# Kernel tuning notes

Hardware: AMD Instinct MI355X
Metric: run time of the kernel (lower is better)

The kernel has to match this reference:

```python
import jax, jax.numpy as jnp
import numpy as np

B, T, IN, H, Z, DH, K = 512, 256, 5, 256, 128, 512, 20
OUT = 6 * K + 3


def setup_inputs() -> dict:
    key = jax.random.key(0)
    ks = jax.random.split(key, 24)
    p = lambda k, shp: jax.random.normal(k, shp, dtype=jnp.float32) * 0.05
    return {
        "s": jax.random.normal(ks[0], (B, T, IN), dtype=jnp.float32),
        "epsilon": jax.random.normal(ks[1], (Z,), dtype=jnp.float32),
        "Wih_f": p(ks[2], (4 * H, IN)), "Whh_f": p(ks[3], (4 * H, H)),
        "bih_f": p(ks[4], (4 * H,)), "bhh_f": p(ks[5], (4 * H,)),
        "Wih_b": p(ks[6], (4 * H, IN)), "Whh_b": p(ks[7], (4 * H, H)),
        "bih_b": p(ks[8], (4 * H,)), "bhh_b": p(ks[9], (4 * H,)),
        "W_sigma": p(ks[10], (Z, 2 * H)), "b_sigma": p(ks[11], (Z,)),
        "W_mu": p(ks[12], (Z, 2 * H)), "b_mu": p(ks[13], (Z,)),
        "W_h0": p(ks[14], (DH, Z)), "b_h0": p(ks[15], (DH,)),
        "Wih_d": p(ks[16], (4 * DH, IN + Z)), "Whh_d": p(ks[17], (4 * DH, DH)),
        "bih_d": p(ks[18], (4 * DH,)), "bhh_d": p(ks[19], (4 * DH,)),
        "W_dec": p(ks[20], (OUT, DH)), "b_dec": p(ks[21], (OUT,)),
    }


def _lstm_scan(x, Wih, Whh, b, reverse):
    # x: [T, B, in]; PyTorch gate order i, f, g, o
    Hh = Whh.shape[1]
    h0 = jnp.zeros((x.shape[1], Hh), x.dtype)

    def step(carry, xt):
        h, c = carry
        g = xt @ Wih.T + h @ Whh.T + b
        i, f, gg, o = jnp.split(g, 4, axis=-1)
        c = jax.nn.sigmoid(f) * c + jax.nn.sigmoid(i) * jnp.tanh(gg)
        h = jax.nn.sigmoid(o) * jnp.tanh(c)
        return (h, c), h

    _, hs = jax.lax.scan(step, (h0, h0), x, reverse=reverse)
    return hs  # [T, B, Hh]


def _mdn(y):
    # y: [..., 123] -> per-mixture (pi, mu1, mu2, sx, sy, corr) + 3 pen logits
    mix = y[..., :6 * K].reshape(y.shape[:-1] + (K, 6))
    pi = jax.nn.softmax(mix[..., 0], axis=-1)
    out_mix = jnp.stack(
        [pi, mix[..., 1], mix[..., 2], jnp.exp(mix[..., 3]),
         jnp.exp(mix[..., 4]), jnp.tanh(mix[..., 5])], axis=-1)
    pen = jax.nn.softmax(y[..., 6 * K:], axis=-1)
    return jnp.concatenate([out_mix.reshape(y.shape[:-1] + (6 * K,)), pen], axis=-1)


def reference(s, epsilon, Wih_f, Whh_f, bih_f, bhh_f, Wih_b, Whh_b, bih_b, bhh_b,
              W_sigma, b_sigma, W_mu, b_mu, W_h0, b_h0,
              Wih_d, Whh_d, bih_d, bhh_d, W_dec, b_dec):
    x = jnp.transpose(s, (1, 0, 2))  # [T, B, 5]
    hf = _lstm_scan(x, Wih_f, Whh_f, bih_f + bhh_f, False)
    hb = _lstm_scan(x, Wih_b, Whh_b, bih_b + bhh_b, True)
    h = jnp.concatenate([hf[-1], hb[-1]], axis=-1)  # output at last time step, [B, 512]
    presig = h @ W_sigma.T + b_sigma
    mu = h @ W_mu.T + b_mu
    sigma = jnp.exp(presig / 2)
    z = mu + sigma * epsilon  # [B, Z]
    h0 = jnp.tanh(z @ W_h0.T + b_h0)
    c0 = jnp.zeros((s.shape[0], DH), s.dtype)
    s0 = jnp.tile(jnp.array([0.0, 0.0, 1.0, 0.0, 0.0], s.dtype), (s.shape[0], 1))
    dec_in = jnp.concatenate([s0[None], x[:T - 1]], axis=0)  # [T, B, 5]
    bdec = bih_d + bhh_d

    def step(carry, st):
        hh, cc = carry
        xt = jnp.concatenate([st, z], axis=-1)  # [B, 133]
        g = xt @ Wih_d.T + hh @ Whh_d.T + bdec
        i, f, gg, o = jnp.split(g, 4, axis=-1)
        cc = jax.nn.sigmoid(f) * cc + jax.nn.sigmoid(i) * jnp.tanh(gg)
        hh = jax.nn.sigmoid(o) * jnp.tanh(cc)
        y = hh @ W_dec.T + b_dec
        return (hh, cc), y

    _, ys = jax.lax.scan(step, (h0, c0), dec_in)  # [T, B, 123]
    output = _mdn(jnp.transpose(ys, (1, 0, 2)))   # [B, T, 123]
    return (output, mu, presig)
```

## Files before the change

### kernel.cpp

```cpp
#include <hip/hip_runtime.h>

typedef unsigned short u16;
typedef unsigned long long u64;
typedef __attribute__((ext_vector_type(8))) short bfrag;
typedef __attribute__((ext_vector_type(4))) float f32x4;

#define MFMA __builtin_amdgcn_mfma_f32_16x16x32_bf16

#define OFF_FLAGS 0ull
#define OFF_HENC  4096ull
#define OFF_WENC  528384ull
#define OFF_WDEC  1118208ull
#define OFF_WY    3870720ull
#define OFF_WMS   4001792ull
#define OFF_WH0   4280320ull
#define OFF_HDEC  4444160ull
#define OFF_HLAT  5492736ull
#define OFF_MS    6049792ull
#define OFF_AZ    6574080ull

__device__ __forceinline__ u16 f2bf(float f) {
  union { float f; unsigned int i; } v; v.f = f;
  unsigned int r = v.i + 0x7fffu + ((v.i >> 16) & 1u);
  return (u16)(r >> 16);
}
__device__ __forceinline__ float sigm(float x) { return 1.0f / (1.0f + __expf(-x)); }
__device__ __forceinline__ float tanh_(float x) {
  float a = fabsf(x);
  float e = __expf(-2.0f * a);
  float r = (1.0f - e) / (1.0f + e);
  return x < 0.0f ? -r : r;
}

__device__ __forceinline__ u64 aload(const u64* p) {
  return __hip_atomic_load(p, __ATOMIC_RELAXED, __HIP_MEMORY_SCOPE_AGENT);
}
__device__ __forceinline__ void astore(u64* p, u64 v) {
  __hip_atomic_store(p, v, __ATOMIC_RELAXED, __HIP_MEMORY_SCOPE_AGENT);
}
__device__ __forceinline__ float afload(const float* p) {
  return __hip_atomic_load(p, __ATOMIC_RELAXED, __HIP_MEMORY_SCOPE_AGENT);
}
__device__ __forceinline__ void afstore(float* p, float v) {
  __hip_atomic_store(p, v, __ATOMIC_RELAXED, __HIP_MEMORY_SCOPE_AGENT);
}

__device__ __forceinline__ void gwait(int* flags, int g, int ep, int tid, int* sdead) {
  if (ep > 0) {
    if (tid < 32 && *sdead == 0) {
      int* fp = flags + g * 64 + tid;
      int spin = 0;
      while (__hip_atomic_load(fp, __ATOMIC_RELAXED, __HIP_MEMORY_SCOPE_AGENT) < ep) {
        __builtin_amdgcn_s_sleep(1);
        if (++spin > (1 << 20)) { *sdead = 1; break; }
      }
    }
  }
  __syncthreads();
  asm volatile("" ::: "memory");
}
__device__ __forceinline__ void garrive(int* flags, int g, int m, int ep, int tid) {
  asm volatile("s_waitcnt vmcnt(0)" ::: "memory");
  __syncthreads();
  if (tid == 0)
    __hip_atomic_store(flags + g * 64 + m, ep, __ATOMIC_RELAXED, __HIP_MEMORY_SCOPE_AGENT);
}

__global__ void pack_wenc(const float* __restrict__ Whh, const float* __restrict__ Wih,
                          const float* __restrict__ bi, const float* __restrict__ bh,
                          u16* __restrict__ out) {
  int idx = blockIdx.x * 256 + threadIdx.x;
  if (idx >= 294912) return;
  int m = idx / 9216, within = idx % 9216;
  int kb = within >> 10, rest = within & 1023;
  int ng = rest >> 9, l = (rest >> 3) & 63, j = rest & 7;
  int nl = ng * 16 + (l & 15);
  int u = nl >> 2, g = nl & 3;
  int row = g * 256 + m * 8 + u;
  int k = kb * 32 + (l >> 4) * 8 + j;
  float v = 0.f;
  if (k < 256) v = Whh[row * 256 + k];
  else if (k < 261) v = Wih[row * 5 + (k - 256)];
  else if (k == 261) v = bi[row] + bh[row];
  out[idx] = f2bf(v);
}

__global__ void pack_wdec(const float* __restrict__ Whh, const float* __restrict__ Wih,
                          const float* __restrict__ bi, const float* __restrict__ bh,
                          u16* __restrict__ out) {
  int idx = blockIdx.x * 256 + threadIdx.x;
  if (idx >= 1376256) return;
  int m = idx / 43008, within = idx % 43008;
  int kb = within >> 11, rest = within & 2047;
  int w = rest >> 9, l = (rest >> 3) & 63, j = rest & 7;
  int nl = w * 16 + (l & 15);
  int u = nl >> 2, g = nl & 3;
  int row = g * 512 + m * 16 + u;
  int k = kb * 32 + (l >> 4) * 8 + j;
  float v = 0.f;
  if (k < 512) v = Whh[row * 512 + k];
  else if (k < 640) v = Wih[row * 133 + 5 + (k - 512)];
  else if (k < 645) v = Wih[row * 133 + (k - 640)];
  else if (k == 645) v = bi[row] + bh[row];
  out[idx] = f2bf(v);
}

__global__ void pack_wy(const float* __restrict__ Wd, u16* __restrict__ out) {
  int idx = blockIdx.x * 256 + threadIdx.x;
  if (idx >= 65536) return;
  int m = idx >> 13, within = idx & 8191;
  int kb = within >> 9, rest = within & 511;
  int l = rest >> 3, j = rest & 7;
  int row = m * 16 + (l & 15);
  int k = kb * 32 + (l >> 4) * 8 + j;
  float v = (row < 123 && k < 512) ? Wd[row * 512 + k] : 0.f;
  out[idx] = f2bf(v);
}

__global__ void pack_wms(const float* __restrict__ Wmu, const float* __restrict__ bmu,
                         const float* __restrict__ Wsig, const float* __restrict__ bsig,
                         u16* __restrict__ out) {
  int idx = blockIdx.x * 256 + threadIdx.x;
  if (idx >= 139264) return;
  int r = idx / 544, k = idx % 544;
  float v = 0.f;
  if (r < 128) {
    if (k < 512) v = Wmu[r * 512 + k];
    else if (k == 512) v = bmu[r];
  } else {
    int r2 = r - 128;
    if (k < 512) v = Wsig[r2 * 512 + k];
    else if (k == 512) v = bsig[r2];
  }
  out[idx] = f2bf(v);
}

__global__ void pack_wh0(const float* __restrict__ Wh0, const float* __restrict__ bh0,
                         u16* __restrict__ out) {
  int idx = blockIdx.x * 256 + threadIdx.x;
  if (idx >= 81920) return;
  int r = idx / 160, k = idx % 160;
  float v = 0.f;
  if (k < 128) v = Wh0[r * 128 + k];
  else if (k == 128) v = bh0[r];
  out[idx] = f2bf(v);
}

__global__ __launch_bounds__(256, 1) void rnn_persist(
    int* __restrict__ flags, u16* __restrict__ henc,
    const u16* __restrict__ WENCP, const u16* __restrict__ WDECP,
    const u16* __restrict__ WYP, const u16* __restrict__ WMSP, const u16* __restrict__ WH0P,
    u16* __restrict__ hdec, u16* __restrict__ hlat, float* __restrict__ msbuf,
    u16* __restrict__ Az,
    const float* __restrict__ s, const float* __restrict__ eps,
    const float* __restrict__ Wih_b, const float* __restrict__ bih_b,
    const float* __restrict__ bhh_b,
    const float* __restrict__ b_dec, float* __restrict__ out)
{
  __shared__ __align__(16) u16 sm[72960];
  __shared__ __align__(16) float gbuf[2112];
  __shared__ __align__(16) u16 hst[1024];
  __shared__ int sdead;

  const int tid = threadIdx.x;
  const int blk = blockIdx.x;
  const int g = blk & 7;
  const int m = blk >> 3;
  const int B0 = g * 64;
  const int w = tid >> 6, l = tid & 63;
  const int lr = l & 15, ko = (l >> 4) * 8;

  float* out_mu = out + 16121856;
  float* out_ps = out + 16187392;

  const int gcol = m * 16 + lr;
  float bd = 0.f;
  if (m < 8 && gcol < 123) bd = b_dec[gcol];

  if (tid == 0) sdead = 0;
  {
    bfrag zz = {0, 0, 0, 0, 0, 0, 0, 0};
    #pragma unroll
    for (int i = 0; i < 5; ++i) {
      int c = i * 256 + tid;
      if (c < 1184) *(bfrag*)(sm + c * 8) = zz;
    }
  }
  {
    const u16* src = WENCP + (size_t)m * 9216;
    #pragma unroll
    for (int i = 0; i < 5; ++i) {
      int c = i * 256 + tid;
      if (c < 1152) *(bfrag*)(sm + 21760 + c * 8) = *(const bfrag*)(src + c * 8);
    }
  }
  __syncthreads();
  if (tid < 32) sm[tid * 296 + 261] = 0x3F80;
  __syncthreads();

  float c_enc0 = 0.f, c_enc1 = 0.f;
  #pragma unroll 1
  for (int t = 0; t < 256; ++t) {
    gwait(flags, g, t, tid, &sdead);
    const u64* hs0 = (const u64*)(henc + (size_t)((t + 1) & 1) * 131072 + (size_t)B0 * 256);
    u64 hv0[8], hv1[8];
    #pragma unroll
    for (int i = 0; i < 8; ++i) hv0[i] = aload(hs0 + i * 256 + tid);
    #pragma unroll
    for (int i = 0; i < 8; ++i) hv1[i] = aload(hs0 + 2048 + i * 256 + tid);
    #pragma unroll
    for (int hh = 0; hh < 2; ++hh) {
      #pragma unroll
      for (int i = 0; i < 8; ++i) {
        int idx = i * 256 + tid;
        *(u64*)(sm + (idx >> 6) * 296 + (idx & 63) * 4) = (hh == 0) ? hv0[i] : hv1[i];
      }
      if (tid < 32) {
        const float* xr = s + ((size_t)(B0 + hh * 32 + tid) * 256 + t) * 5;
        #pragma unroll
        for (int j = 0; j < 5; ++j) sm[tid * 296 + 256 + j] = f2bf(xr[j]);
      }
      __syncthreads();
      const int mt = w >> 1, ng = w & 1;
      f32x4 acc = {0.f, 0.f, 0.f, 0.f};
      #pragma unroll
      for (int kb = 0; kb < 9; ++kb) {
        bfrag a = *(const bfrag*)(sm + (mt * 16 + lr) * 296 + kb * 32 + ko);
        bfrag bw = *(const bfrag*)(sm + 21760 + (kb * 2 + ng) * 512 + l * 8);
        acc = MFMA(a, bw, acc, 0, 0, 0);
      }
      #pragma unroll
      for (int j = 0; j < 4; ++j)
        gbuf[(mt * 16 + (l >> 4) * 4 + j) * 33 + ng * 16 + lr] = acc[j];
      __syncthreads();
      {
        int bl = tid >> 3, u = tid & 7;
        float gi = gbuf[bl * 33 + u * 4 + 0], gf = gbuf[bl * 33 + u * 4 + 1];
        float gg = gbuf[bl * 33 + u * 4 + 2], go = gbuf[bl * 33 + u * 4 + 3];
        float cprev = (hh == 0) ? c_enc0 : c_enc1;
        float c = sigm(gf) * cprev + sigm(gi) * tanh_(gg);
        if (hh == 0) c_enc0 = c; else c_enc1 = c;
        hst[bl * 8 + u] = f2bf(sigm(go) * tanh_(c));
      }
      __syncthreads();
      if (tid < 64) {
        int row = tid >> 1, q = tid & 1;
        u64 v = *(const u64*)(hst + row * 8 + q * 4);
        astore((u64*)(henc + (size_t)(t & 1) * 131072 + (size_t)(B0 + hh * 32 + row) * 256 + m * 8) + q, v);
      }
    }
    garrive(flags, g, m, t + 1, tid);
  }

  u16* lat_hf = (u16*)gbuf;
  u16* lat_hb = (u16*)gbuf + 512;
  u16* lat_z  = (u16*)gbuf + 1024;

  gwait(flags, g, 256, tid, &sdead);
  {
    const u16* src = WDECP + (size_t)m * 43008;
    #pragma unroll 1
    for (int i = 0; i < 21; ++i) {
      int c = i * 256 + tid;
      *(bfrag*)(sm + 21760 + c * 8) = *(const bfrag*)(src + c * 8);
    }
  }
  if (m < 8) {
    const u16* src = WYP + (size_t)m * 8192;
    #pragma unroll
    for (int i = 0; i < 4; ++i) {
      int c = i * 256 + tid;
      *(bfrag*)(sm + 64768 + c * 8) = *(const bfrag*)(src + c * 8);
    }
  }
  #pragma unroll
  for (int r = 0; r < 2; ++r) {
    int b = B0 + m * 2 + r;
    if (tid < 64) {
      u64 v = aload((const u64*)(henc + 131072 + (size_t)b * 256) + tid);
      *(u64*)(lat_hf + r * 256 + tid * 4) = v;
    }
    {
      const float* xr = s + ((size_t)b * 256 + 255) * 5;
      float x0 = xr[0], x1 = xr[1], x2 = xr[2], x3 = xr[3], x4 = xr[4];
      int n = tid;
      float gv[4];
      #pragma unroll
      for (int gg = 0; gg < 4; ++gg) {
        int row = gg * 256 + n;
        gv[gg] = bih_b[row] + bhh_b[row] + x0 * Wih_b[row * 5] + x1 * Wih_b[row * 5 + 1] +
                 x2 * Wih_b[row * 5 + 2] + x3 * Wih_b[row * 5 + 3] + x4 * Wih_b[row * 5 + 4];
      }
      float c = sigm(gv[0]) * tanh_(gv[2]);
      lat_hb[r * 256 + n] = f2bf(sigm(gv[3]) * tanh_(c));
    }
  }
  __syncthreads();
  #pragma unroll
  for (int it = 0; it < 2; ++it) {
    int idx = it * 256 + tid;
    if (idx < 272) {
      int rr = idx / 136, u = idx % 136;
      u64 pv = 0;
      #pragma unroll
      for (int q = 0; q < 4; ++q) {
        int c = u * 4 + q;
        u16 x;
        if (c < 256) x = lat_hf[rr * 256 + c];
        else if (c < 512) x = lat_hb[rr * 256 + c - 256];
        else if (c == 512) x = 0x3F80;
        else x = 0;
        pv |= ((u64)x) << (q * 16);
      }
      astore((u64*)(hlat + (size_t)(B0 + m * 2 + rr) * 544) + u, pv);
    }
  }
  garrive(flags, g, m, 257, tid);

  gwait(flags, g, 257, tid, &sdead);
  {
    const int bH = m >> 4, cT = m & 15;
    const u64* src = (const u64*)(hlat + (size_t)(B0 + bH * 32) * 544);
    u64 sv[17];
    #pragma unroll
    for (int i = 0; i < 17; ++i) sv[i] = aload(src + i * 256 + tid);
    #pragma unroll
    for (int i = 0; i < 17; ++i) *(u64*)(sm + (i * 256 + tid) * 4) = sv[i];
    __syncthreads();
    if (w < 2) {
      f32x4 acc = {0.f, 0.f, 0.f, 0.f};
      const u16* bp = WMSP + (size_t)(cT * 16 + lr) * 544 + ko;
      #pragma unroll
      for (int kb = 0; kb < 17; ++kb) {
        bfrag a = *(const bfrag*)(sm + (w * 16 + lr) * 544 + kb * 32 + ko);
        bfrag bb = *(const bfrag*)(bp + kb * 32);
        acc = MFMA(a, bb, acc, 0, 0, 0);
      }
      int nc = cT * 16 + lr;
      #pragma unroll
      for (int j = 0; j < 4; ++j) {
        int b = B0 + bH * 32 + w * 16 + (l >> 4) * 4 + j;
        afstore(msbuf + (size_t)b * 256 + nc, acc[j]);
        if (nc < 128) out_mu[(size_t)b * 128 + nc] = acc[j];
        else out_ps[(size_t)b * 128 + nc - 128] = acc[j];
      }
    }
  }
  garrive(flags, g, m, 258, tid);

  gwait(flags, g, 258, tid, &sdead);
  {
    int r = tid >> 7, zj = tid & 127;
    int b = B0 + m * 2 + r;
    float mu = afload(msbuf + (size_t)b * 256 + zj);
    float ps = afload(msbuf + (size_t)b * 256 + 128 + zj);
    float z = mu + __expf(0.5f * ps) * eps[zj];
    lat_z[r * 128 + zj] = f2bf(z);
  }
  __syncthreads();
  if (tid < 80) {
    int r = tid / 40, u = tid % 40;
    u64 pv = 0;
    #pragma unroll
    for (int q = 0; q < 4; ++q) {
      int c = u * 4 + q;
      u16 x;
      if (c < 128) x = lat_z[r * 128 + c];
      else if (c == 128) x = 0x3F80;
      else x = 0;
      pv |= ((u64)x) << (q * 16);
    }
    astore((u64*)(Az + (size_t)(B0 + m * 2 + r) * 160) + u, pv);
  }
  garrive(flags, g, m, 259, tid);

  gwait(flags, g, 259, tid, &sdead);
  u64 zreg0[4], zreg1[4];
  {
    int r = tid >> 3;
    #pragma unroll
    for (int i = 0; i < 4; ++i) {
      int uu = (tid & 7) * 4 + i;
      zreg0[i] = aload((const u64*)(Az + (size_t)(B0 + r) * 160) + uu);
      zreg1[i] = aload((const u64*)(Az + (size_t)(B0 + 32 + r) * 160) + uu);
    }
  }
  {
    const u64* src = (const u64*)(Az + (size_t)B0 * 160);
    u64 sv[10];
    #pragma unroll
    for (int i = 0; i < 10; ++i) sv[i] = aload(src + i * 256 + tid);
    #pragma unroll
    for (int i = 0; i < 10; ++i) *(u64*)(sm + (i * 256 + tid) * 4) = sv[i];
    __syncthreads();
    f32x4 acc = {0.f, 0.f, 0.f, 0.f};
    const u16* bp = WH0P + (size_t)(m * 16 + lr) * 160 + ko;
    #pragma unroll
    for (int kb = 0; kb < 5; ++kb) {
      bfrag a = *(const bfrag*)(sm + (w * 16 + lr) * 160 + kb * 32 + ko);
      bfrag bb = *(const bfrag*)(bp + kb * 32);
      acc = MFMA(a, bb, acc, 0, 0, 0);
    }
    #pragma unroll
    for (int j = 0; j < 4; ++j)
      hst[(w * 16 + (l >> 4) * 4 + j) * 16 + lr] = f2bf(tanh_(acc[j]));
  }
  __syncthreads();
  #pragma unroll
  for (int i = 0; i < 5; ++i) {
    int idx = i * 256 + tid;
    if (idx < 1120) {
      int row = idx / 35, c = idx % 35;
      sm[row * 680 + 645 + c] = (c == 0) ? 0x3F80 : 0;
    }
  }
  {
    int row = tid >> 2, q = tid & 3;
    u64 v = *(const u64*)(hst + row * 16 + q * 4);
    astore((u64*)(hdec + 262144 + (size_t)(B0 + row) * 512 + m * 16) + q, v);
  }
  garrive(flags, g, m, 260, tid);

  float c_dec00 = 0.f, c_dec01 = 0.f, c_dec10 = 0.f, c_dec11 = 0.f;
  #pragma unroll 1
  for (int t = 0; t < 256; ++t) {
    gwait(flags, g, 260 + t, tid, &sdead);
    const u64* hs0 = (const u64*)(hdec + (size_t)((t + 1) & 1) * 262144 + (size_t)B0 * 512);
    u64 hv0[16], hv1[16];
    #pragma unroll
    for (int i = 0; i < 16; ++i) hv0[i] = aload(hs0 + i * 256 + tid);
    #pragma unroll
    for (int i = 0; i < 16; ++i) hv1[i] = aload(hs0 + 4096 + i * 256 + tid);
    #pragma unroll
    for (int hh = 0; hh < 2; ++hh) {
      #pragma unroll
      for (int i = 0; i < 16; ++i) {
        int idx = i * 256 + tid;
        *(u64*)(sm + (idx >> 7) * 680 + (idx & 127) * 4) = (hh == 0) ? hv0[i] : hv1[i];
      }
      {
        int r = tid >> 3;
        #pragma unroll
        for (int i = 0; i < 4; ++i) {
          int uu = (tid & 7) * 4 + i;
          *(u64*)(sm + r * 680 + 512 + uu * 4) = (hh == 0) ? zreg0[i] : zreg1[i];
        }
      }
      if (tid < 32) {
        if (t == 0) {
          sm[tid * 680 + 640] = 0; sm[tid * 680 + 641] = 0; sm[tid * 680 + 642] = 0x3F80;
          sm[tid * 680 + 643] = 0; sm[tid * 680 + 644] = 0;
        } else {
          const float* xr = s + ((size_t)(B0 + hh * 32 + tid) * 256 + (t - 1)) * 5;
          #pragma unroll
          for (int j = 0; j < 5; ++j) sm[tid * 680 + 640 + j] = f2bf(xr[j]);
        }
      }
      __syncthreads();
      const int mtd = w & 1, nb = (w >> 1) * 2;
      const bool doy = (m < 8) && (w < 2) && (t > 0);
      f32x4 acc0 = {0.f, 0.f, 0.f, 0.f}, acc1 = {0.f, 0.f, 0.f, 0.f}, accy = {0.f, 0.f, 0.f, 0.f};
      #pragma unroll
      for (int kb = 0; kb < 21; ++kb) {
        bfrag a  = *(const bfrag*)(sm + (mtd * 16 + lr) * 680 + kb * 32 + ko);
        bfrag b0 = *(const bfrag*)(sm + 21760 + kb * 2048 + nb * 512 + l * 8);
        bfrag b1 = *(const bfrag*)(sm + 21760 + kb * 2048 + (nb + 1) * 512 + l * 8);
        acc0 = MFMA(a, b0, acc0, 0, 0, 0);
        acc1 = MFMA(a, b1, acc1, 0, 0, 0);
        if (kb < 16 && doy) {
          bfrag by = *(const bfrag*)(sm + 64768 + kb * 512 + l * 8);
          accy = MFMA(a, by, accy, 0, 0, 0);
        }
      }
      if (doy && gcol < 123) {
        int brow = B0 + hh * 32 + w * 16 + (l >> 4) * 4;
        #pragma unroll
        for (int j = 0; j < 4; ++j)
          out[((size_t)(brow + j) * 256 + (t - 1)) * 123 + gcol] = accy[j] + bd;
      }
      #pragma unroll
      for (int j = 0; j < 4; ++j) {
        int grow = mtd * 16 + (l >> 4) * 4 + j;
        gbuf[grow * 66 + nb * 16 + lr] = acc0[j];
        gbuf[grow * 66 + (nb + 1) * 16 + lr] = acc1[j];
      }
      __syncthreads();
      #pragma unroll
      for (int p = 0; p < 2; ++p) {
        int idx = p * 256 + tid;
        int bl = idx >> 4, u = idx & 15;
        float gi = gbuf[bl * 66 + u * 4 + 0], gf = gbuf[bl * 66 + u * 4 + 1];
        float gg = gbuf[bl * 66 + u * 4 + 2], go = gbuf[bl * 66 + u * 4 + 3];
        float cprev = (hh == 0) ? (p == 0 ? c_dec00 : c_dec01) : (p == 0 ? c_dec10 : c_dec11);
        float c = sigm(gf) * cprev + sigm(gi) * tanh_(gg);
        if (hh == 0) { if (p == 0) c_dec00 = c; else c_dec01 = c; }
        else         { if (p == 0) c_dec10 = c; else c_dec11 = c; }
        hst[bl * 16 + u] = f2bf(sigm(go) * tanh_(c));
      }
      __syncthreads();
      if (tid < 128) {
        int row = tid >> 2, q = tid & 3;
        u64 v = *(const u64*)(hst + row * 16 + q * 4);
        astore((u64*)(hdec + (size_t)(t & 1) * 262144 + (size_t)(B0 + hh * 32 + row) * 512 + m * 16) + q, v);
      }
    }
    garrive(flags, g, m, 261 + t, tid);
  }

  gwait(flags, g, 516, tid, &sdead);
  #pragma unroll
  for (int hh = 0; hh < 2; ++hh) {
    const u64* hsrc = (const u64*)(hdec + 262144 + (size_t)(B0 + hh * 32) * 512);
    u64 hv[16];
    #pragma unroll
    for (int i = 0; i < 16; ++i) hv[i] = aload(hsrc + i * 256 + tid);
    #pragma unroll
    for (int i = 0; i < 16; ++i) {
      int idx = i * 256 + tid;
      *(u64*)(sm + (idx >> 7) * 680 + (idx & 127) * 4) = hv[i];
    }
    __syncthreads();
    if (m < 8 && w < 2) {
      f32x4 accy = {0.f, 0.f, 0.f, 0.f};
      #pragma unroll
      for (int kb = 0; kb < 16; ++kb) {
        bfrag a = *(const bfrag*)(sm + (w * 16 + lr) * 680 + kb * 32 + ko);
        bfrag by = *(const bfrag*)(sm + 64768 + kb * 512 + l * 8);
        accy = MFMA(a, by, accy, 0, 0, 0);
      }
      if (gcol < 123) {
        int brow = B0 + hh * 32 + w * 16 + (l >> 4) * 4;
        #pragma unroll
        for (int j = 0; j < 4; ++j)
          out[((size_t)(brow + j) * 256 + 255) * 123 + gcol] = accy[j] + bd;
      }
    }
    __syncthreads();
  }
}

__global__ __launch_bounds__(64) void mdn_final(float* __restrict__ out) {
  __shared__ float rows[64 * 123];
  const int tid = threadIdx.x;
  float4* g4 = (float4*)(out + (size_t)blockIdx.x * 64 * 123);
  #pragma unroll
  for (int i = 0; i < 31; ++i) {
    int c = i * 64 + tid;
    if (c < 1968) ((float4*)rows)[c] = g4[c];
  }
  __syncthreads();
  {
    float* r = rows + tid * 123;
    float m1 = -1e30f;
    #pragma unroll
    for (int k = 0; k < 20; ++k) m1 = fmaxf(m1, r[6 * k]);
    float s1 = 0.f;
    #pragma unroll
    for (int k = 0; k < 20; ++k) s1 += __expf(r[6 * k] - m1);
    float i1 = 1.f / s1;
    #pragma unroll
    for (int k = 0; k < 20; ++k) {
      r[6 * k] = __expf(r[6 * k] - m1) * i1;
      r[6 * k + 3] = __expf(r[6 * k + 3]);
      r[6 * k + 4] = __expf(r[6 * k + 4]);
      r[6 * k + 5] = tanh_(r[6 * k + 5]);
    }
    float p0 = r[120], p1 = r[121], p2 = r[122];
    float mp = fmaxf(p0, fmaxf(p1, p2));
    float e0 = __expf(p0 - mp), e1 = __expf(p1 - mp), e2 = __expf(p2 - mp);
    float ip = 1.f / (e0 + e1 + e2);
    r[120] = e0 * ip; r[121] = e1 * ip; r[122] = e2 * ip;
  }
  __syncthreads();
  #pragma unroll
  for (int i = 0; i < 31; ++i) {
    int c = i * 64 + tid;
    if (c < 1968) g4[c] = ((float4*)rows)[c];
  }
}

extern "C" void kernel_launch(void* const* d_in, const int* in_sizes, int n_in,
                              void* d_out, int out_size, void* d_ws, size_t ws_size,
                              hipStream_t stream) {
  const float* s       = (const float*)d_in[0];
  const float* eps     = (const float*)d_in[1];
  const float* Wih_f   = (const float*)d_in[2];
  const float* Whh_f   = (const float*)d_in[3];
  const float* bih_f   = (const float*)d_in[4];
  const float* bhh_f   = (const float*)d_in[5];
  const float* Wih_b   = (const float*)d_in[6];
  const float* bih_b   = (const float*)d_in[8];
  const float* bhh_b   = (const float*)d_in[9];
  const float* W_sigma = (const float*)d_in[10];
  const float* b_sigma = (const float*)d_in[11];
  const float* W_mu    = (const float*)d_in[12];
  const float* b_mu    = (const float*)d_in[13];
  const float* W_h0    = (const float*)d_in[14];
  const float* b_h0    = (const float*)d_in[15];
  const float* Wih_d   = (const float*)d_in[16];
  const float* Whh_d   = (const float*)d_in[17];
  const float* bih_d   = (const float*)d_in[18];
  const float* bhh_d   = (const float*)d_in[19];
  const float* W_dec   = (const float*)d_in[20];
  const float* b_dec   = (const float*)d_in[21];

  char* ws = (char*)d_ws;
  int* FLAGS  = (int*)(ws + OFF_FLAGS);
  u16* HENC   = (u16*)(ws + OFF_HENC);
  u16* WENCP  = (u16*)(ws + OFF_WENC);
  u16* WDECP  = (u16*)(ws + OFF_WDEC);
  u16* WYP    = (u16*)(ws + OFF_WY);
  u16* WMSP   = (u16*)(ws + OFF_WMS);
  u16* WH0P   = (u16*)(ws + OFF_WH0);
  u16* HDEC   = (u16*)(ws + OFF_HDEC);
  u16* HLAT   = (u16*)(ws + OFF_HLAT);
  float* MS   = (float*)(ws + OFF_MS);
  u16* AZ     = (u16*)(ws + OFF_AZ);
  float* out  = (float*)d_out;

  hipMemsetAsync(ws, 0, 4096 + 524288, stream);

  pack_wenc<<<1152, 256, 0, stream>>>(Whh_f, Wih_f, bih_f, bhh_f, WENCP);
  pack_wdec<<<5376, 256, 0, stream>>>(Whh_d, Wih_d, bih_d, bhh_d, WDECP);
  pack_wy<<<256, 256, 0, stream>>>(W_dec, WYP);
  pack_wms<<<544, 256, 0, stream>>>(W_mu, b_mu, W_sigma, b_sigma, WMSP);
  pack_wh0<<<320, 256, 0, stream>>>(W_h0, b_h0, WH0P);

  rnn_persist<<<256, 256, 0, stream>>>(FLAGS, HENC, WENCP, WDECP, WYP, WMSP, WH0P,
                                       HDEC, HLAT, MS, AZ, s, eps,
                                       Wih_b, bih_b, bhh_b, b_dec, out);

  mdn_final<<<2048, 64, 0, stream>>>(out);

  (void)in_sizes; (void)n_in; (void)out_size; (void)ws_size;
}
```

Measured before the change: 2.984 ms.

## Split per-group barrier into two half-batch flags and prepack bf16 inputs

The cross-block barrier for each batch group is split into two independent flag sets, one per 32-row half. Each half can wait, compute and arrive on its own, so one half's sync latency can overlap the other half's compute in both the encoder and decoder recurrences. A new pre-kernel packs the input sequence into bf16 rows of 8 with a bias-one column, replacing per-step scalar fp32 loads and conversions with single 64-bit loads. The mu/sigma scratch buffer is dropped in favour of reading the output arrays directly, and the spin timeout is shortened, which adds flag-ordering complexity and some risk of deadlock-detection misfires.

```diff
diff --git a/kernel.cpp b/kernel.cpp
--- a/kernel.cpp
+++ b/kernel.cpp
@@ -16,8 +16,8 @@
 #define OFF_WH0   4280320ull
 #define OFF_HDEC  4444160ull
 #define OFF_HLAT  5492736ull
-#define OFF_MS    6049792ull
-#define OFF_AZ    6574080ull
+#define OFF_AZ    6049792ull
+#define OFF_SX    6213632ull
 
 __device__ __forceinline__ u16 f2bf(float f) {
   union { float f; unsigned int i; } v; v.f = f;
@@ -45,25 +45,25 @@
   __hip_atomic_store(p, v, __ATOMIC_RELAXED, __HIP_MEMORY_SCOPE_AGENT);
 }
 
-__device__ __forceinline__ void gwait(int* flags, int g, int ep, int tid, int* sdead) {
+__device__ __forceinline__ void gwait(int* base, int ep, int tid, int* sdead) {
   if (ep > 0) {
     if (tid < 32 && *sdead == 0) {
-      int* fp = flags + g * 64 + tid;
+      int* fp = base + tid;
       int spin = 0;
       while (__hip_atomic_load(fp, __ATOMIC_RELAXED, __HIP_MEMORY_SCOPE_AGENT) < ep) {
         __builtin_amdgcn_s_sleep(1);
-        if (++spin > (1 << 20)) { *sdead = 1; break; }
+        if (++spin > (1 << 18)) { *sdead = 1; break; }
       }
     }
   }
   __syncthreads();
   asm volatile("" ::: "memory");
 }
-__device__ __forceinline__ void garrive(int* flags, int g, int m, int ep, int tid) {
+__device__ __forceinline__ void garrive(int* base, int m, int ep, int tid) {
   asm volatile("s_waitcnt vmcnt(0)" ::: "memory");
   __syncthreads();
   if (tid == 0)
-    __hip_atomic_store(flags + g * 64 + m, ep, __ATOMIC_RELAXED, __HIP_MEMORY_SCOPE_AGENT);
+    __hip_atomic_store(base + m, ep, __ATOMIC_RELAXED, __HIP_MEMORY_SCOPE_AGENT);
 }
 
 __global__ void pack_wenc(const float* __restrict__ Whh, const float* __restrict__ Wih,
@@ -146,12 +146,22 @@
   out[idx] = f2bf(v);
 }
 
+__global__ void pack_sx(const float* __restrict__ s, u16* __restrict__ out) {
+  int idx = blockIdx.x * 256 + threadIdx.x;
+  if (idx >= 1048576) return;
+  int j = idx & 7, b = (idx >> 3) & 511, t = idx >> 12;
+  u16 v;
+  if (j < 5) v = f2bf(s[((size_t)b * 256 + t) * 5 + j]);
+  else v = (j == 5) ? (u16)0x3F80 : (u16)0;
+  out[idx] = v;
+}
+
 __global__ __launch_bounds__(256, 1) void rnn_persist(
     int* __restrict__ flags, u16* __restrict__ henc,
     const u16* __restrict__ WENCP, const u16* __restrict__ WDECP,
     const u16* __restrict__ WYP, const u16* __restrict__ WMSP, const u16* __restrict__ WH0P,
-    u16* __restrict__ hdec, u16* __restrict__ hlat, float* __restrict__ msbuf,
-    u16* __restrict__ Az,
+    u16* __restrict__ hdec, u16* __restrict__ hlat, u16* __restrict__ Az,
+    const u16* __restrict__ SXD,
     const float* __restrict__ s, const float* __restrict__ eps,
     const float* __restrict__ Wih_b, const float* __restrict__ bih_b,
     const float* __restrict__ bhh_b,
@@ -169,6 +179,8 @@
   const int B0 = g * 64;
   const int w = tid >> 6, l = tid & 63;
   const int lr = l & 15, ko = (l >> 4) * 8;
+  int* FA = flags + g * 128;
+  int* FB = FA + 64;
 
   float* out_mu = out + 16121856;
   float* out_ps = out + 16187392;
@@ -195,30 +207,28 @@
     }
   }
   __syncthreads();
-  if (tid < 32) sm[tid * 296 + 261] = 0x3F80;
-  __syncthreads();
 
   float c_enc0 = 0.f, c_enc1 = 0.f;
   #pragma unroll 1
   for (int t = 0; t < 256; ++t) {
-    gwait(flags, g, t, tid, &sdead);
-    const u64* hs0 = (const u64*)(henc + (size_t)((t + 1) & 1) * 131072 + (size_t)B0 * 256);
-    u64 hv0[8], hv1[8];
-    #pragma unroll
-    for (int i = 0; i < 8; ++i) hv0[i] = aload(hs0 + i * 256 + tid);
-    #pragma unroll
-    for (int i = 0; i < 8; ++i) hv1[i] = aload(hs0 + 2048 + i * 256 + tid);
-    #pragma unroll
-    for (int hh = 0; hh < 2; ++hh) {
+    #pragma unroll
+    for (int X = 0; X < 2; ++X) {
+      int* F = X ? FB : FA;
+      gwait(F, t, tid, &sdead);
+      const u64* hs = (const u64*)(henc + (size_t)((t + 1) & 1) * 131072 +
+                                   (size_t)(B0 + X * 32) * 256);
+      u64 hv[8];
+      #pragma unroll
+      for (int i = 0; i < 8; ++i) hv[i] = aload(hs + i * 256 + tid);
       #pragma unroll
       for (int i = 0; i < 8; ++i) {
         int idx = i * 256 + tid;
-        *(u64*)(sm + (idx >> 6) * 296 + (idx & 63) * 4) = (hh == 0) ? hv0[i] : hv1[i];
-      }
-      if (tid < 32) {
-        const float* xr = s + ((size_t)(B0 + hh * 32 + tid) * 256 + t) * 5;
-        #pragma unroll
-        for (int j = 0; j < 5; ++j) sm[tid * 296 + 256 + j] = f2bf(xr[j]);
+        *(u64*)(sm + (idx >> 6) * 296 + (idx & 63) * 4) = hv[i];
+      }
+      if (tid < 64) {
+        int row = tid >> 1, q = tid & 1;
+        *(u64*)(sm + row * 296 + 256 + q * 4) =
+            *(const u64*)(SXD + ((size_t)(t * 512 + B0 + X * 32 + row)) * 8 + q * 4);
       }
       __syncthreads();
       const int mt = w >> 1, ng = w & 1;
@@ -237,26 +247,28 @@
         int bl = tid >> 3, u = tid & 7;
         float gi = gbuf[bl * 33 + u * 4 + 0], gf = gbuf[bl * 33 + u * 4 + 1];
         float gg = gbuf[bl * 33 + u * 4 + 2], go = gbuf[bl * 33 + u * 4 + 3];
-        float cprev = (hh == 0) ? c_enc0 : c_enc1;
+        float cprev = (X == 0) ? c_enc0 : c_enc1;
         float c = sigm(gf) * cprev + sigm(gi) * tanh_(gg);
-        if (hh == 0) c_enc0 = c; else c_enc1 = c;
+        if (X == 0) c_enc0 = c; else c_enc1 = c;
         hst[bl * 8 + u] = f2bf(sigm(go) * tanh_(c));
       }
       __syncthreads();
       if (tid < 64) {
         int row = tid >> 1, q = tid & 1;
         u64 v = *(const u64*)(hst + row * 8 + q * 4);
-        astore((u64*)(henc + (size_t)(t & 1) * 131072 + (size_t)(B0 + hh * 32 + row) * 256 + m * 8) + q, v);
-      }
-    }
-    garrive(flags, g, m, t + 1, tid);
+        astore((u64*)(henc + (size_t)(t & 1) * 131072 +
+                      (size_t)(B0 + X * 32 + row) * 256 + m * 8) + q, v);
+      }
+      garrive(F, m, t + 1, tid);
+    }
   }
 
   u16* lat_hf = (u16*)gbuf;
   u16* lat_hb = (u16*)gbuf + 512;
   u16* lat_z  = (u16*)gbuf + 1024;
 
-  gwait(flags, g, 256, tid, &sdead);
+  gwait(FA, 256, tid, &sdead);
+  gwait(FB, 256, tid, &sdead);
   {
     const u16* src = WDECP + (size_t)m * 43008;
     #pragma unroll 1
@@ -315,9 +327,9 @@
       astore((u64*)(hlat + (size_t)(B0 + m * 2 + rr) * 544) + u, pv);
     }
   }
-  garrive(flags, g, m, 257, tid);
-
-  gwait(flags, g, 257, tid, &sdead);
+  garrive(FA, m, 257, tid);
+
+  gwait(FA, 257, tid, &sdead);
   {
     const int bH = m >> 4, cT = m & 15;
     const u64* src = (const u64*)(hlat + (size_t)(B0 + bH * 32) * 544);
@@ -340,20 +352,19 @@
       #pragma unroll
       for (int j = 0; j < 4; ++j) {
         int b = B0 + bH * 32 + w * 16 + (l >> 4) * 4 + j;
-        afstore(msbuf + (size_t)b * 256 + nc, acc[j]);
-        if (nc < 128) out_mu[(size_t)b * 128 + nc] = acc[j];
-        else out_ps[(size_t)b * 128 + nc - 128] = acc[j];
-      }
-    }
-  }
-  garrive(flags, g, m, 258, tid);
-
-  gwait(flags, g, 258, tid, &sdead);
+        if (nc < 128) afstore(out_mu + (size_t)b * 128 + nc, acc[j]);
+        else afstore(out_ps + (size_t)b * 128 + nc - 128, acc[j]);
+      }
+    }
+  }
+  garrive(FA, m, 258, tid);
+
+  gwait(FA, 258, tid, &sdead);
   {
     int r = tid >> 7, zj = tid & 127;
     int b = B0 + m * 2 + r;
-    float mu = afload(msbuf + (size_t)b * 256 + zj);
-    float ps = afload(msbuf + (size_t)b * 256 + 128 + zj);
+    float mu = afload(out_mu + (size_t)b * 128 + zj);
+    float ps = afload(out_ps + (size_t)b * 128 + zj);
     float z = mu + __expf(0.5f * ps) * eps[zj];
     lat_z[r * 128 + zj] = f2bf(z);
   }
@@ -372,9 +383,9 @@
     }
     astore((u64*)(Az + (size_t)(B0 + m * 2 + r) * 160) + u, pv);
   }
-  garrive(flags, g, m, 259, tid);
-
-  gwait(flags, g, 259, tid, &sdead);
+  garrive(FA, m, 259, tid);
+
+  gwait(FA, 259, tid, &sdead);
   u64 zreg0[4], zreg1[4];
   {
     int r = tid >> 3;
@@ -419,42 +430,42 @@
     u64 v = *(const u64*)(hst + row * 16 + q * 4);
     astore((u64*)(hdec + 262144 + (size_t)(B0 + row) * 512 + m * 16) + q, v);
   }
-  garrive(flags, g, m, 260, tid);
+  garrive(FA, m, 260, tid);
+  if (tid == 0)
+    __hip_atomic_store(FB + m, 257, __ATOMIC_RELAXED, __HIP_MEMORY_SCOPE_AGENT);
 
   float c_dec00 = 0.f, c_dec01 = 0.f, c_dec10 = 0.f, c_dec11 = 0.f;
   #pragma unroll 1
   for (int t = 0; t < 256; ++t) {
-    gwait(flags, g, 260 + t, tid, &sdead);
-    const u64* hs0 = (const u64*)(hdec + (size_t)((t + 1) & 1) * 262144 + (size_t)B0 * 512);
-    u64 hv0[16], hv1[16];
-    #pragma unroll
-    for (int i = 0; i < 16; ++i) hv0[i] = aload(hs0 + i * 256 + tid);
-    #pragma unroll
-    for (int i = 0; i < 16; ++i) hv1[i] = aload(hs0 + 4096 + i * 256 + tid);
-    #pragma unroll
-    for (int hh = 0; hh < 2; ++hh) {
+    #pragma unroll
+    for (int X = 0; X < 2; ++X) {
+      int* F = X ? FB : FA;
+      int base = X ? 257 : 260;
+      gwait(F, base + t, tid, &sdead);
+      const u64* hs = (const u64*)(hdec + (size_t)((t + 1) & 1) * 262144 +
+                                   (size_t)(B0 + X * 32) * 512);
+      u64 hv[16];
+      #pragma unroll
+      for (int i = 0; i < 16; ++i) hv[i] = aload(hs + i * 256 + tid);
       #pragma unroll
       for (int i = 0; i < 16; ++i) {
         int idx = i * 256 + tid;
-        *(u64*)(sm + (idx >> 7) * 680 + (idx & 127) * 4) = (hh == 0) ? hv0[i] : hv1[i];
+        *(u64*)(sm + (idx >> 7) * 680 + (idx & 127) * 4) = hv[i];
       }
       {
         int r = tid >> 3;
         #pragma unroll
         for (int i = 0; i < 4; ++i) {
           int uu = (tid & 7) * 4 + i;
-          *(u64*)(sm + r * 680 + 512 + uu * 4) = (hh == 0) ? zreg0[i] : zreg1[i];
+          *(u64*)(sm + r * 680 + 512 + uu * 4) = (X == 0) ? zreg0[i] : zreg1[i];
         }
       }
-      if (tid < 32) {
-        if (t == 0) {
-          sm[tid * 680 + 640] = 0; sm[tid * 680 + 641] = 0; sm[tid * 680 + 642] = 0x3F80;
-          sm[tid * 680 + 643] = 0; sm[tid * 680 + 644] = 0;
-        } else {
-          const float* xr = s + ((size_t)(B0 + hh * 32 + tid) * 256 + (t - 1)) * 5;
-          #pragma unroll
-          for (int j = 0; j < 5; ++j) sm[tid * 680 + 640 + j] = f2bf(xr[j]);
-        }
+      if (tid < 64) {
+        int row = tid >> 1, q = tid & 1;
+        u64 v;
+        if (t == 0) v = q ? 0x000000003F800000ULL : 0x00003F8000000000ULL;
+        else v = *(const u64*)(SXD + ((size_t)((t - 1) * 512 + B0 + X * 32 + row)) * 8 + q * 4);
+        *(u64*)(sm + row * 680 + 640 + q * 4) = v;
       }
       __syncthreads();
       const int mtd = w & 1, nb = (w >> 1) * 2;
@@ -473,7 +484,7 @@
         }
       }
       if (doy && gcol < 123) {
-        int brow = B0 + hh * 32 + w * 16 + (l >> 4) * 4;
+        int brow = B0 + X * 32 + w * 16 + (l >> 4) * 4;
         #pragma unroll
         for (int j = 0; j < 4; ++j)
           out[((size_t)(brow + j) * 256 + (t - 1)) * 123 + gcol] = accy[j] + bd;
@@ -491,26 +502,28 @@
         int bl = idx >> 4, u = idx & 15;
         float gi = gbuf[bl * 66 + u * 4 + 0], gf = gbuf[bl * 66 + u * 4 + 1];
         float gg = gbuf[bl * 66 + u * 4 + 2], go = gbuf[bl * 66 + u * 4 + 3];
-        float cprev = (hh == 0) ? (p == 0 ? c_dec00 : c_dec01) : (p == 0 ? c_dec10 : c_dec11);
+        float cprev = (X == 0) ? (p == 0 ? c_dec00 : c_dec01) : (p == 0 ? c_dec10 : c_dec11);
         float c = sigm(gf) * cprev + sigm(gi) * tanh_(gg);
-        if (hh == 0) { if (p == 0) c_dec00 = c; else c_dec01 = c; }
-        else         { if (p == 0) c_dec10 = c; else c_dec11 = c; }
+        if (X == 0) { if (p == 0) c_dec00 = c; else c_dec01 = c; }
+        else        { if (p == 0) c_dec10 = c; else c_dec11 = c; }
         hst[bl * 16 + u] = f2bf(sigm(go) * tanh_(c));
       }
       __syncthreads();
       if (tid < 128) {
         int row = tid >> 2, q = tid & 3;
         u64 v = *(const u64*)(hst + row * 16 + q * 4);
-        astore((u64*)(hdec + (size_t)(t & 1) * 262144 + (size_t)(B0 + hh * 32 + row) * 512 + m * 16) + q, v);
-      }
-    }
-    garrive(flags, g, m, 261 + t, tid);
-  }
-
-  gwait(flags, g, 516, tid, &sdead);
+        astore((u64*)(hdec + (size_t)(t & 1) * 262144 +
+                      (size_t)(B0 + X * 32 + row) * 512 + m * 16) + q, v);
+      }
+      garrive(F, m, base + t + 1, tid);
+    }
+  }
+
+  gwait(FA, 516, tid, &sdead);
+  gwait(FB, 513, tid, &sdead);
   #pragma unroll
-  for (int hh = 0; hh < 2; ++hh) {
-    const u64* hsrc = (const u64*)(hdec + 262144 + (size_t)(B0 + hh * 32) * 512);
+  for (int X = 0; X < 2; ++X) {
+    const u64* hsrc = (const u64*)(hdec + 262144 + (size_t)(B0 + X * 32) * 512);
     u64 hv[16];
     #pragma unroll
     for (int i = 0; i < 16; ++i) hv[i] = aload(hsrc + i * 256 + tid);
@@ -529,7 +542,7 @@
         accy = MFMA(a, by, accy, 0, 0, 0);
       }
       if (gcol < 123) {
-        int brow = B0 + hh * 32 + w * 16 + (l >> 4) * 4;
+        int brow = B0 + X * 32 + w * 16 + (l >> 4) * 4;
         #pragma unroll
         for (int j = 0; j < 4; ++j)
           out[((size_t)(brow + j) * 256 + 255) * 123 + gcol] = accy[j] + bd;
@@ -614,8 +627,8 @@
   u16* WH0P   = (u16*)(ws + OFF_WH0);
   u16* HDEC   = (u16*)(ws + OFF_HDEC);
   u16* HLAT   = (u16*)(ws + OFF_HLAT);
-  float* MS   = (float*)(ws + OFF_MS);
   u16* AZ     = (u16*)(ws + OFF_AZ);
+  u16* SXD    = (u16*)(ws + OFF_SX);
   float* out  = (float*)d_out;
 
   hipMemsetAsync(ws, 0, 4096 + 524288, stream);
@@ -625,9 +638,10 @@
   pack_wy<<<256, 256, 0, stream>>>(W_dec, WYP);
   pack_wms<<<544, 256, 0, stream>>>(W_mu, b_mu, W_sigma, b_sigma, WMSP);
   pack_wh0<<<320, 256, 0, stream>>>(W_h0, b_h0, WH0P);
+  pack_sx<<<4096, 256, 0, stream>>>(s, SXD);
 
   rnn_persist<<<256, 256, 0, stream>>>(FLAGS, HENC, WENCP, WDECP, WYP, WMSP, WH0P,
-                                       HDEC, HLAT, MS, AZ, s, eps,
+                                       HDEC, HLAT, AZ, SXD, s, eps,
                                        Wih_b, bih_b, bhh_b, b_dec, out);
 
   mdn_final<<<2048, 64, 0, stream>>>(out);
```

New measurement: 2.991 ms. No clear change (+0.3%).
